# Optimization experiments

Hardware: AMD Instinct MI355X
Metric: run time of the kernel (lower is better)

Reference implementation:

```python
import jax, jax.numpy as jnp
import numpy as np

D, H, DH = 768, 12, 64
W = 256            # one-sided window (attention_window=512 total)
EPS = 1e-6
NEG = -1e9


def layer_norm(x, g, b):
    m = jnp.mean(x, axis=-1, keepdims=True)
    v = jnp.mean((x - m) ** 2, axis=-1, keepdims=True)
    return g * (x - m) * jax.lax.rsqrt(v + EPS) + b


def _blocks3(t, nb):
    # t: [B,H,nb,W,dh] -> keys/values of 3 neighboring blocks [B,H,nb,3W,dh]
    tp = jnp.pad(t, ((0, 0), (0, 0), (1, 1), (0, 0), (0, 0)))
    return jnp.concatenate([tp[:, :, :nb], tp[:, :, 1:nb + 1], tp[:, :, 2:nb + 2]], axis=3)


def sliding_window_attention(x, kpm, Wq, bq, Wk, bk, Wv, bv, Wo, bo):
    B, S, _ = x.shape
    nb = S // W
    def proj(Wm, bm):
        return (x @ Wm + bm).reshape(B, S, H, DH).transpose(0, 2, 1, 3).reshape(B, H, nb, W, DH)
    q = proj(Wq, bq) * (1.0 / np.sqrt(DH))
    k = proj(Wk, bk)
    v = proj(Wv, bv)
    k3 = _blocks3(k, nb)
    v3 = _blocks3(v, nb)
    # scores over local band: [B,H,nb,W,3W]
    s = jnp.einsum('bhnqd,bhnkd->bhnqk', q, k3)
    qi = jnp.arange(W)[:, None]
    kj = jnp.arange(3 * W)[None, :]
    band = jnp.abs(kj - W - qi) <= W                     # [W,3W]
    kg = (jnp.arange(nb)[:, None, None] - 1) * W + kj[None]  # global key idx [nb,1,3W]
    inrange = (kg >= 0) & (kg < S)
    # key padding mask gathered into block layout: [B,nb,3W]
    kpm_b = jnp.pad(kpm.reshape(B, nb, W), ((0, 0), (1, 1), (0, 0)), constant_values=True)
    kpm3 = jnp.concatenate([kpm_b[:, :nb], kpm_b[:, 1:nb + 1], kpm_b[:, 2:nb + 2]], axis=2)
    m = band[None, None, None] & inrange[None, None] & (~kpm3)[:, None, :, None, :]
    s = jnp.where(m, s, NEG)
    p = jax.nn.softmax(s, axis=-1)
    o = jnp.einsum('bhnqk,bhnkd->bhnqd', p, v3)
    o = o.reshape(B, H, S, DH).transpose(0, 2, 1, 3).reshape(B, S, D)
    return o @ Wo + bo


def setup_inputs() -> dict:
    key = jax.random.key(0)
    ks = jax.random.split(key, 12)
    B, S, DF = 2, 4096, 3072
    sc = 1.0 / np.sqrt(D)
    return {
        'x': jax.random.normal(ks[0], (B, S, D), jnp.float32),
        'mask': jnp.zeros((B, S), bool),
        'id': 0,
        'Wq': jax.random.normal(ks[1], (D, D), jnp.float32) * sc,
        'bq': jnp.zeros((D,), jnp.float32),
        'Wk': jax.random.normal(ks[2], (D, D), jnp.float32) * sc,
        'bk': jnp.zeros((D,), jnp.float32),
        'Wv': jax.random.normal(ks[3], (D, D), jnp.float32) * sc,
        'bv': jnp.zeros((D,), jnp.float32),
        'Wo': jax.random.normal(ks[4], (D, D), jnp.float32) * sc,
        'bo': jnp.zeros((D,), jnp.float32),
        'ln1_g': jnp.ones((D,), jnp.float32),
        'ln1_b': jnp.zeros((D,), jnp.float32),
        'W1': jax.random.normal(ks[5], (D, DF), jnp.float32) * sc,
        'b1': jnp.zeros((DF,), jnp.float32),
        'W2': jax.random.normal(ks[6], (DF, D), jnp.float32) * (1.0 / np.sqrt(DF)),
        'b2': jnp.zeros((D,), jnp.float32),
        'ln2_g': jnp.ones((D,), jnp.float32),
        'ln2_b': jnp.zeros((D,), jnp.float32),
    }


def reference(x, mask, id, Wq, bq, Wk, bk, Wv, bv, Wo, bo, ln1_g, ln1_b, W1, b1, W2, b2, ln2_g, ln2_b):
    # Sublayer 1: pre-norm residual around sliding-window self-attention
    h = layer_norm(x, ln1_g, ln1_b)
    x = x + sliding_window_attention(h, mask, Wq, bq, Wk, bk, Wv, bv, Wo, bo)
    # Sublayer 2: pre-norm residual around positionwise FFN
    h = layer_norm(x, ln2_g, ln2_b)
    x = x + (jax.nn.relu(h @ W1 + b1) @ W2 + b2)
    return x
```

## Files before the change

### kernel.cpp

```cpp
#include <hip/hip_runtime.h>
#include <hip/hip_bf16.h>
#include <cstddef>

typedef __attribute__((ext_vector_type(8))) short short8;
typedef __attribute__((ext_vector_type(4))) float f32x4;
typedef __attribute__((ext_vector_type(4))) unsigned short us4;

typedef __attribute__((address_space(1))) void as1_void;
typedef __attribute__((address_space(3))) void as3_void;

__device__ __forceinline__ void gload16(const void* g, void* lds) {
  __builtin_amdgcn_global_load_lds((as1_void*)(void*)g, (as3_void*)lds, 16, 0, 0);
}

__device__ inline unsigned short f2bf(float f) {
  union { float f; unsigned int u; } v; v.f = f;
  return (unsigned short)((v.u + 0x7FFFu + ((v.u >> 16) & 1u)) >> 16);
}

__device__ __forceinline__ float exp2v(float x) {
  float r; asm("v_exp_f32 %0, %1" : "=v"(r) : "v"(x)); return r;
}
__device__ __forceinline__ unsigned cvtpk(float a, float b) {
  unsigned r; asm("v_cvt_pk_bf16_f32 %0, %1, %2" : "=v"(r) : "v"(a), "v"(b)); return r;
}

__global__ __launch_bounds__(256) void ln_kernel(const float* __restrict__ x,
    const float* __restrict__ g, const float* __restrict__ b,
    unsigned short* __restrict__ out)
{
  int row = blockIdx.x, t = threadIdx.x;
  const float* xr = x + (size_t)row * 768;
  float v0 = xr[t], v1 = xr[t + 256], v2 = xr[t + 512];
  float s = v0 + v1 + v2;
  #pragma unroll
  for (int o = 32; o > 0; o >>= 1) s += __shfl_xor(s, o);
  __shared__ float r1[4], r2[4];
  if ((t & 63) == 0) r1[t >> 6] = s;
  __syncthreads();
  float mean = (r1[0] + r1[1] + r1[2] + r1[3]) * (1.0f / 768.0f);
  float d0 = v0 - mean, d1 = v1 - mean, d2 = v2 - mean;
  float q = d0 * d0 + d1 * d1 + d2 * d2;
  #pragma unroll
  for (int o = 32; o > 0; o >>= 1) q += __shfl_xor(q, o);
  if ((t & 63) == 0) r2[t >> 6] = q;
  __syncthreads();
  float var = (r2[0] + r2[1] + r2[2] + r2[3]) * (1.0f / 768.0f);
  float rs = rsqrtf(var + 1e-6f);
  unsigned short* orow = out + (size_t)row * 768;
  orow[t]       = f2bf(g[t]       * d0 * rs + b[t]);
  orow[t + 256] = f2bf(g[t + 256] * d1 * rs + b[t + 256]);
  orow[t + 512] = f2bf(g[t + 512] * d2 * rs + b[t + 512]);
}

__global__ __launch_bounds__(256) void transpose_kernel(const float* __restrict__ W,
    unsigned short* __restrict__ WT, int K, int N)
{
  __shared__ float tile[32][33];
  int tx = threadIdx.x & 31, ty = threadIdx.x >> 5;
  int k0 = blockIdx.x * 32, n0 = blockIdx.y * 32;
  #pragma unroll
  for (int i = 0; i < 32; i += 8)
    tile[ty + i][tx] = W[(size_t)(k0 + ty + i) * N + n0 + tx];
  __syncthreads();
  #pragma unroll
  for (int i = 0; i < 32; i += 8)
    WT[(size_t)(n0 + ty + i) * K + k0 + tx] = f2bf(tile[tx][ty + i]);
}

__global__ __launch_bounds__(256) void catbias_kernel(const float* __restrict__ bq,
    const float* __restrict__ bk, const float* __restrict__ bv, float* __restrict__ o)
{
  int i = blockIdx.x * 256 + threadIdx.x;
  o[i] = (i < 768) ? bq[i] : ((i < 1536) ? bk[i - 768] : bv[i - 1536]);
}

enum { EPI_QKV = 0, EPI_RELU = 1, EPI_RESID = 2 };

template<int EPI>
__global__ __launch_bounds__(512, 1) void gemmP_kernel(
    const unsigned short* __restrict__ A, const unsigned short* __restrict__ BT,
    const float* __restrict__ bias, const float* __restrict__ resid,
    void* __restrict__ outp, int M, int N, int K, int ntn)
{
  __shared__ char lds[3][49152];
  int tid = threadIdx.x;
  int nwg = gridDim.x;
  int bid = ((int)blockIdx.x & 7) * (nwg >> 3) + ((int)blockIdx.x >> 3);
  int mt = bid / ntn, nt = bid % ntn;
  int m0 = mt * 128, n0 = nt * 256;
  int w = tid >> 6, l = tid & 63;
  int wr = w >> 2, wc = w & 3;
  int fr = l & 15, fq = l >> 4;
  int swz = (fr >> 1) * 128 + (((((fr & 1) << 2) | fq) ^ ((fr >> 1) & 7)) << 4);
  int t8 = tid >> 3;
  int uu = (tid & 7) ^ (t8 & 7);
  int rb = 2 * t8 + (uu >> 2);
  int kb = (uu & 3) * 8;
  const unsigned short* Asrc  = A  + (size_t)(m0 + rb) * K + kb;
  const unsigned short* Bsrc0 = BT + (size_t)(n0 + rb) * K + kb;
  const unsigned short* Bsrc1 = BT + (size_t)(n0 + 128 + rb) * K + kb;

  auto stage = [&](int buf, int kt, int h) {
    int ko = kt * 64 + h * 32;
    char* dA = &lds[buf][0] + h * 8192 + (w << 10);
    char* dB = &lds[buf][16384] + h * 16384 + (w << 10);
    gload16(Asrc + ko, dA);
    gload16(Bsrc0 + ko, dB);
    gload16(Bsrc1 + ko, dB + 8192);
  };

  f32x4 acc[4][4] = {};

#define GP_COMPUTE(RBUF, H)                                                    \
  { short8 af[4], bf[4];                                                       \
    const char* ab_ = &lds[RBUF][0] + (H) * 8192 + wr * 4096 + swz;            \
    const char* bb_ = &lds[RBUF][16384] + (H) * 16384 + wc * 4096 + swz;       \
    _Pragma("unroll")                                                          \
    for (int i_ = 0; i_ < 4; i_++) af[i_] = *(const short8*)(ab_ + i_ * 1024); \
    _Pragma("unroll")                                                          \
    for (int j_ = 0; j_ < 4; j_++) bf[j_] = *(const short8*)(bb_ + j_ * 1024); \
    __builtin_amdgcn_s_setprio(1);                                             \
    _Pragma("unroll")                                                          \
    for (int i_ = 0; i_ < 4; i_++)                                             \
      _Pragma("unroll")                                                        \
      for (int j_ = 0; j_ < 4; j_++)                                           \
        acc[i_][j_] = __builtin_amdgcn_mfma_f32_16x16x32_bf16(                 \
            af[i_], bf[j_], acc[i_][j_], 0, 0, 0);                             \
    __builtin_amdgcn_s_setprio(0); }

  stage(0, 0, 0); stage(0, 0, 1); stage(1, 1, 0); stage(1, 1, 1);
  asm volatile("s_waitcnt vmcnt(9)" ::: "memory");
  __builtin_amdgcn_s_barrier();

  int NT = K >> 6;
  int R = 0;
  for (int t = 0; t < NT - 2; ++t) {
    int W = (R == 0) ? 2 : R - 1;
    stage(W, t + 2, 0);
    GP_COMPUTE(R, 0);
    asm volatile("s_waitcnt vmcnt(9)" ::: "memory");
    __builtin_amdgcn_s_barrier();
    stage(W, t + 2, 1);
    GP_COMPUTE(R, 1);
    asm volatile("s_waitcnt vmcnt(9)" ::: "memory");
    __builtin_amdgcn_s_barrier();
    R = (R == 2) ? 0 : R + 1;
  }
  GP_COMPUTE(R, 0);
  asm volatile("s_waitcnt vmcnt(6)" ::: "memory");
  __builtin_amdgcn_s_barrier();
  GP_COMPUTE(R, 1);
  asm volatile("s_waitcnt vmcnt(3)" ::: "memory");
  __builtin_amdgcn_s_barrier();
  R = (R == 2) ? 0 : R + 1;
  GP_COMPUTE(R, 0);
  asm volatile("s_waitcnt vmcnt(0)" ::: "memory");
  __builtin_amdgcn_s_barrier();
  GP_COMPUTE(R, 1);
#undef GP_COMPUTE

  #pragma unroll
  for (int nj = 0; nj < 4; nj++) {
    int col = n0 + wc * 64 + nj * 16 + fr;
    float bs = bias[col];
    if (EPI == EPI_QKV) {
      int which = (col >= 1536) ? 2 : ((col >= 768) ? 1 : 0);
      int c2 = col - which * 768;
      int hh = c2 >> 6, dh = c2 & 63;
      if (which == 2) {
        unsigned short* dstv = reinterpret_cast<unsigned short*>(outp) + (size_t)2 * 8192 * 768;
        #pragma unroll
        for (int i = 0; i < 4; i++) {
          int row0 = m0 + wr * 64 + i * 16 + fq * 4;
          int bb = row0 >> 12, sl = row0 & 4095;
          us4 pv;
          #pragma unroll
          for (int r = 0; r < 4; r++) pv[r] = f2bf(acc[i][nj][r] + bs);
          *reinterpret_cast<us4*>(&dstv[((size_t)(bb * 12 + hh) * 64 + dh) * 4096 + sl]) = pv;
        }
      } else {
        unsigned short* dst = reinterpret_cast<unsigned short*>(outp) + (size_t)which * 8192 * 768;
        #pragma unroll
        for (int i = 0; i < 4; i++) {
          #pragma unroll
          for (int r = 0; r < 4; r++) {
            int row = m0 + wr * 64 + i * 16 + fq * 4 + r;
            float c = acc[i][nj][r] + bs;
            if (which == 0) c *= 0.18033688011112042f;
            int bb = row >> 12, sl = row & 4095;
            dst[(((size_t)(bb * 12 + hh)) * 4096 + sl) * 64 + dh] = f2bf(c);
          }
        }
      }
    } else if (EPI == EPI_RELU) {
      #pragma unroll
      for (int i = 0; i < 4; i++)
        #pragma unroll
        for (int r = 0; r < 4; r++) {
          int row = m0 + wr * 64 + i * 16 + fq * 4 + r;
          float c = fmaxf(acc[i][nj][r] + bs, 0.0f);
          reinterpret_cast<unsigned short*>(outp)[(size_t)row * N + col] = f2bf(c);
        }
    } else {
      #pragma unroll
      for (int i = 0; i < 4; i++)
        #pragma unroll
        for (int r = 0; r < 4; r++) {
          int row = m0 + wr * 64 + i * 16 + fq * 4 + r;
          float c = acc[i][nj][r] + bs + resid[(size_t)row * N + col];
          reinterpret_cast<float*>(outp)[(size_t)row * N + col] = c;
        }
    }
  }
}

__global__ __launch_bounds__(256) void attn_fused_kernel(
    const unsigned short* __restrict__ qg, const unsigned short* __restrict__ kg,
    const unsigned short* __restrict__ vtg, const unsigned char* __restrict__ kpm,
    unsigned short* __restrict__ attn_out)
{
  __shared__ unsigned short lds_k[2][64 * 64];
  __shared__ unsigned short lds_vt[2][64 * 64];
  __shared__ unsigned short lds_p[4][32 * 64];
  int bid0 = blockIdx.x;
  int bid = (bid0 & 7) * 96 + (bid0 >> 3);
  int qblk = bid & 31, h = (bid >> 5) % 12, b = bid / 384;
  int bh = b * 12 + h;
  int q0 = qblk * 128;
  int tid = threadIdx.x, w = tid >> 6, l = tid & 63;
  int fr = l & 15, fq = l >> 4;
  int qw0 = q0 + w * 32;
  int swzb = (((l & 7) ^ (l >> 3)) << 4);
  const char* qbase  = (const char*)(qg  + (size_t)bh * 4096 * 64);
  const char* kbase  = (const char*)(kg  + (size_t)bh * 4096 * 64);
  const char* vtbase = (const char*)(vtg + (size_t)bh * 64 * 4096);
  const unsigned char* kpmb = kpm + (size_t)b * 4096;

  #pragma unroll
  for (int s = 0; s < 4; s++) {
    int row = w * 32 + s * 8 + (l >> 3);
    gload16(qbase + (size_t)(q0 + row) * 128 + swzb, (char*)lds_p[w] + s * 1024);
  }

  auto stageKV = [&](int c, int buf) {
    int g0 = q0 - 256 + c * 64;
    if (g0 < 0 || g0 >= 4096) return;
    #pragma unroll
    for (int s = 0; s < 2; s++) {
      int row = w * 16 + s * 8 + (l >> 3);
      gload16(kbase + (size_t)(g0 + row) * 128 + swzb,
              (char*)lds_k[buf] + (w * 2 + s) * 1024);
      gload16(vtbase + ((size_t)row * 4096 + g0) * 2 + swzb,
              (char*)lds_vt[buf] + (w * 2 + s) * 1024);
    }
  };

  stageKV(0, 0);
  asm volatile("s_waitcnt vmcnt(0)");
  __syncthreads();

  short8 qf[2][2];
  #pragma unroll
  for (int i = 0; i < 2; i++)
    #pragma unroll
    for (int ks = 0; ks < 2; ks++)
      qf[i][ks] = *(const short8*)((const char*)lds_p[w] + (i * 16 + fr) * 128 +
                    ((ks * 64 + fq * 16) ^ ((fr & 7) << 4)));

  f32x4 acc_o[2][4] = {};
  float m_st[2] = {-3.0e38f, -3.0e38f};
  float l_st[2] = {0.0f, 0.0f};

  for (int c = 0; c < 10; c++) {
    int g0 = q0 - 256 + c * 64;
    bool valid = (g0 >= 0) && (g0 < 4096);
    if (c < 9) stageKV(c + 1, (c + 1) & 1);
    if (valid) {
      int buf = c & 1;
      unsigned int km[4];
      #pragma unroll
      for (int j = 0; j < 4; j++)
        km[j] = *(const unsigned int*)(kpmb + g0 + 16 * j + 4 * fq);
      bool anyk = __any((km[0] | km[1] | km[2] | km[3]) != 0);
      int rel = g0 - qw0;
      bool edge = anyk || (rel < -225) || (rel > 193);
      short8 kf[4][2];
      #pragma unroll
      for (int j = 0; j < 4; j++)
        #pragma unroll
        for (int ks = 0; ks < 2; ks++)
          kf[j][ks] = *(const short8*)((const char*)lds_k[buf] + (j * 16 + fr) * 128 +
                        ((ks * 64 + fq * 16) ^ ((fr & 7) << 4)));
      f32x4 accs[4][2] = {};
      #pragma unroll
      for (int j = 0; j < 4; j++)
        #pragma unroll
        for (int i = 0; i < 2; i++)
          #pragma unroll
          for (int ks = 0; ks < 2; ks++)
            accs[j][i] = __builtin_amdgcn_mfma_f32_16x16x32_bf16(kf[j][ks], qf[i][ks], accs[j][i], 0, 0, 0);
      #pragma unroll
      for (int i = 0; i < 2; i++) {
        float sv[4][4];
        #pragma unroll
        for (int j = 0; j < 4; j++)
          #pragma unroll
          for (int r = 0; r < 4; r++)
            sv[j][r] = accs[j][i][r];
        if (edge) {
          int base = rel + 4 * fq - fr - 16 * i;
          #pragma unroll
          for (int j = 0; j < 4; j++)
            #pragma unroll
            for (int r = 0; r < 4; r++) {
              int d = base + 16 * j + r;
              bool ok = (d >= -256) && (d <= 256) && (((km[j] >> (8 * r)) & 255u) == 0u);
              if (!ok) sv[j][r] = -1.0e9f;
            }
        }
        float mv = sv[0][0];
        #pragma unroll
        for (int j = 0; j < 4; j++)
          #pragma unroll
          for (int r = 0; r < 4; r++) mv = fmaxf(mv, sv[j][r]);
        mv = fmaxf(mv, __shfl_xor(mv, 16));
        mv = fmaxf(mv, __shfl_xor(mv, 32));
        float mo = m_st[i];
        if (!__all(mv - mo <= 8.0f)) {
          float mn = fmaxf(mo, mv);
          float scl = exp2v(mo - mn);
          l_st[i] *= scl;
          m_st[i] = mn;
          #pragma unroll
          for (int r = 0; r < 4; r++) {
            float so = __shfl(scl, (l & 48) | ((l >> 2) & 12) | r);
            #pragma unroll
            for (int jd = 0; jd < 4; jd++) acc_o[i][jd][r] *= so;
          }
        }
        float mn = m_st[i];
        float rs = 0.0f;
        char* prow = (char*)lds_p[w] + (i * 16 + fr) * 128;
        #pragma unroll
        for (int j = 0; j < 4; j++) {
          float p0 = exp2v(sv[j][0] - mn), p1 = exp2v(sv[j][1] - mn);
          float p2 = exp2v(sv[j][2] - mn), p3 = exp2v(sv[j][3] - mn);
          rs += (p0 + p1) + (p2 + p3);
          uint2 u; u.x = cvtpk(p0, p1); u.y = cvtpk(p2, p3);
          *(uint2*)(prow + ((32 * j + 8 * fq) ^ ((fr & 7) << 4))) = u;
        }
        rs += __shfl_xor(rs, 16);
        rs += __shfl_xor(rs, 32);
        l_st[i] += rs;
      }
      short8 pf[2][2];
      #pragma unroll
      for (int i = 0; i < 2; i++)
        #pragma unroll
        for (int ks = 0; ks < 2; ks++)
          pf[i][ks] = *(const short8*)((const char*)lds_p[w] + (i * 16 + fr) * 128 +
                        ((ks * 64 + fq * 16) ^ ((fr & 7) << 4)));
      short8 vf[4][2];
      #pragma unroll
      for (int jd = 0; jd < 4; jd++)
        #pragma unroll
        for (int ks = 0; ks < 2; ks++)
          vf[jd][ks] = *(const short8*)((const char*)lds_vt[buf] + (jd * 16 + fr) * 128 +
                        ((ks * 64 + fq * 16) ^ ((fr & 7) << 4)));
      #pragma unroll
      for (int i = 0; i < 2; i++)
        #pragma unroll
        for (int jd = 0; jd < 4; jd++)
          #pragma unroll
          for (int ks = 0; ks < 2; ks++)
            acc_o[i][jd] = __builtin_amdgcn_mfma_f32_16x16x32_bf16(pf[i][ks], vf[jd][ks], acc_o[i][jd], 0, 0, 0);
    }
    asm volatile("s_waitcnt vmcnt(0)");
    __syncthreads();
  }
  #pragma unroll
  for (int i = 0; i < 2; i++) {
    #pragma unroll
    for (int r = 0; r < 4; r++) {
      float lv = __shfl(l_st[i], (l & 48) | ((l >> 2) & 12) | r);
      float inv = 1.0f / lv;
      int qrow = qw0 + i * 16 + fq * 4 + r;
      size_t orow = ((size_t)b * 4096 + qrow) * 768 + h * 64;
      #pragma unroll
      for (int jd = 0; jd < 4; jd++)
        attn_out[orow + jd * 16 + fr] = f2bf(acc_o[i][jd][r] * inv);
    }
  }
}

extern "C" void kernel_launch(void* const* d_in, const int* in_sizes, int n_in,
                              void* d_out, int out_size, void* d_ws, size_t ws_size,
                              hipStream_t stream) {
  const float* x            = (const float*)d_in[0];
  const unsigned char* mask = (const unsigned char*)d_in[1];
  const float* Wq  = (const float*)d_in[3];
  const float* bq  = (const float*)d_in[4];
  const float* Wk  = (const float*)d_in[5];
  const float* bk  = (const float*)d_in[6];
  const float* Wv  = (const float*)d_in[7];
  const float* bv  = (const float*)d_in[8];
  const float* Wo  = (const float*)d_in[9];
  const float* bo  = (const float*)d_in[10];
  const float* ln1g = (const float*)d_in[11];
  const float* ln1b = (const float*)d_in[12];
  const float* W1  = (const float*)d_in[13];
  const float* b1  = (const float*)d_in[14];
  const float* W2  = (const float*)d_in[15];
  const float* b2  = (const float*)d_in[16];
  const float* ln2g = (const float*)d_in[17];
  const float* ln2b = (const float*)d_in[18];
  float* out = (float*)d_out;

  char* ws = (char*)d_ws;
  size_t off = 0;
  auto alloc = [&](size_t bytes) -> void* {
    void* p = ws + off;
    off += (bytes + 255) & ~(size_t)255;
    return p;
  };
  unsigned short* WTqkv = (unsigned short*)alloc((size_t)2304 * 768 * 2);
  unsigned short* WTo   = (unsigned short*)alloc((size_t)768 * 768 * 2);
  unsigned short* W1T   = (unsigned short*)alloc((size_t)3072 * 768 * 2);
  unsigned short* W2T   = (unsigned short*)alloc((size_t)768 * 3072 * 2);
  float*          bqkv  = (float*)alloc(2304 * 4);
  unsigned short* hbuf  = (unsigned short*)alloc((size_t)8192 * 768 * 2);
  unsigned short* qkv   = (unsigned short*)alloc((size_t)3 * 8192 * 768 * 2);
  unsigned short* attn  = (unsigned short*)alloc((size_t)8192 * 768 * 2);
  float* x1             = (float*)alloc((size_t)8192 * 768 * 4);
  unsigned short* h2    = (unsigned short*)alloc((size_t)8192 * 768 * 2);
  unsigned short* a1    = (unsigned short*)alloc((size_t)8192 * 3072 * 2);

  transpose_kernel<<<dim3(24, 24), 256, 0, stream>>>(Wq, WTqkv, 768, 768);
  transpose_kernel<<<dim3(24, 24), 256, 0, stream>>>(Wk, WTqkv + (size_t)768 * 768, 768, 768);
  transpose_kernel<<<dim3(24, 24), 256, 0, stream>>>(Wv, WTqkv + (size_t)1536 * 768, 768, 768);
  transpose_kernel<<<dim3(24, 24), 256, 0, stream>>>(Wo, WTo, 768, 768);
  transpose_kernel<<<dim3(24, 96), 256, 0, stream>>>(W1, W1T, 768, 3072);
  transpose_kernel<<<dim3(96, 24), 256, 0, stream>>>(W2, W2T, 3072, 768);
  catbias_kernel<<<9, 256, 0, stream>>>(bq, bk, bv, bqkv);

  ln_kernel<<<8192, 256, 0, stream>>>(x, ln1g, ln1b, hbuf);

  gemmP_kernel<EPI_QKV><<<576, 512, 0, stream>>>(hbuf, WTqkv, bqkv, nullptr, qkv, 8192, 2304, 768, 9);

  attn_fused_kernel<<<768, 256, 0, stream>>>(qkv, qkv + (size_t)8192 * 768,
                                             qkv + (size_t)2 * 8192 * 768, mask, attn);

  gemmP_kernel<EPI_RESID><<<192, 512, 0, stream>>>(attn, WTo, bo, x, x1, 8192, 768, 768, 3);
  ln_kernel<<<8192, 256, 0, stream>>>(x1, ln2g, ln2b, h2);
  gemmP_kernel<EPI_RELU><<<768, 512, 0, stream>>>(h2, W1T, b1, nullptr, a1, 8192, 3072, 768, 12);
  gemmP_kernel<EPI_RESID><<<192, 512, 0, stream>>>(a1, W2T, b2, x1, out, 8192, 768, 3072, 3);
}
```

Baseline: 265.8 us.

## Merge weight prep launches and deepen attention and GEMM prefetch pipelines

Merges the six weight transpose launches and the bias concat into one prep kernel, which removes six launches. The GEMM main loop is reorganised so each phase waits, reads its LDS fragments, issues the next global-to-LDS stage, then barriers before the MFMAs. This lets the loads overlap with compute more cleanly, at the cost of an extra barrier per phase. The attention kernel moves from double to triple buffering of K/V tiles with vmcnt-based waits, removing the full vmcnt(0) wait plus syncthreads at the end of each chunk. It adds LDS use and relies on the vmcnt counting being correct.

```diff
diff --git a/kernel.cpp b/kernel.cpp
--- a/kernel.cpp
+++ b/kernel.cpp
@@ -53,12 +53,33 @@
   orow[t + 512] = f2bf(g[t + 512] * d2 * rs + b[t + 512]);
 }
 
-__global__ __launch_bounds__(256) void transpose_kernel(const float* __restrict__ W,
-    unsigned short* __restrict__ WT, int K, int N)
+__global__ __launch_bounds__(256) void prep_kernel(
+    const float* __restrict__ Wq, const float* __restrict__ Wk,
+    const float* __restrict__ Wv, const float* __restrict__ Wo,
+    const float* __restrict__ W1, const float* __restrict__ W2,
+    const float* __restrict__ bq, const float* __restrict__ bk,
+    const float* __restrict__ bv,
+    unsigned short* __restrict__ WTqkv, unsigned short* __restrict__ WTo,
+    unsigned short* __restrict__ W1T, unsigned short* __restrict__ W2T,
+    float* __restrict__ bqkv)
 {
+  int bid = blockIdx.x;
+  if (bid >= 6912) {
+    int i = (bid - 6912) * 256 + threadIdx.x;
+    bqkv[i] = (i < 768) ? bq[i] : ((i < 1536) ? bk[i - 768] : bv[i - 1536]);
+    return;
+  }
+  const float* W; unsigned short* WT; int K, N, lb;
+  if (bid < 576)       { W = Wq; WT = WTqkv;                        K = 768;  N = 768;  lb = bid; }
+  else if (bid < 1152) { W = Wk; WT = WTqkv + (size_t)768 * 768;    K = 768;  N = 768;  lb = bid - 576; }
+  else if (bid < 1728) { W = Wv; WT = WTqkv + (size_t)1536 * 768;   K = 768;  N = 768;  lb = bid - 1152; }
+  else if (bid < 2304) { W = Wo; WT = WTo;                          K = 768;  N = 768;  lb = bid - 1728; }
+  else if (bid < 4608) { W = W1; WT = W1T;                          K = 768;  N = 3072; lb = bid - 2304; }
+  else                 { W = W2; WT = W2T;                          K = 3072; N = 768;  lb = bid - 4608; }
+  int ntN = N >> 5;
+  int k0 = (lb / ntN) * 32, n0 = (lb % ntN) * 32;
   __shared__ float tile[32][33];
   int tx = threadIdx.x & 31, ty = threadIdx.x >> 5;
-  int k0 = blockIdx.x * 32, n0 = blockIdx.y * 32;
   #pragma unroll
   for (int i = 0; i < 32; i += 8)
     tile[ty + i][tx] = W[(size_t)(k0 + ty + i) * N + n0 + tx];
@@ -66,13 +87,6 @@
   #pragma unroll
   for (int i = 0; i < 32; i += 8)
     WT[(size_t)(n0 + ty + i) * K + k0 + tx] = f2bf(tile[tx][ty + i]);
-}
-
-__global__ __launch_bounds__(256) void catbias_kernel(const float* __restrict__ bq,
-    const float* __restrict__ bk, const float* __restrict__ bv, float* __restrict__ o)
-{
-  int i = blockIdx.x * 256 + threadIdx.x;
-  o[i] = (i < 768) ? bq[i] : ((i < 1536) ? bk[i - 768] : bv[i - 1536]);
 }
 
 enum { EPI_QKV = 0, EPI_RELU = 1, EPI_RESID = 2 };
@@ -111,54 +125,53 @@
   };
 
   f32x4 acc[4][4] = {};
-
-#define GP_COMPUTE(RBUF, H)                                                    \
-  { short8 af[4], bf[4];                                                       \
-    const char* ab_ = &lds[RBUF][0] + (H) * 8192 + wr * 4096 + swz;            \
+  short8 af[4], bf[4];
+
+#define GP_READ(RBUF, H)                                                       \
+  { const char* ab_ = &lds[RBUF][0] + (H) * 8192 + wr * 4096 + swz;            \
     const char* bb_ = &lds[RBUF][16384] + (H) * 16384 + wc * 4096 + swz;       \
     _Pragma("unroll")                                                          \
     for (int i_ = 0; i_ < 4; i_++) af[i_] = *(const short8*)(ab_ + i_ * 1024); \
     _Pragma("unroll")                                                          \
-    for (int j_ = 0; j_ < 4; j_++) bf[j_] = *(const short8*)(bb_ + j_ * 1024); \
-    __builtin_amdgcn_s_setprio(1);                                             \
+    for (int j_ = 0; j_ < 4; j_++) bf[j_] = *(const short8*)(bb_ + j_ * 1024); }
+
+#define GP_MFMA                                                                \
+  __builtin_amdgcn_s_setprio(1);                                               \
+  _Pragma("unroll")                                                            \
+  for (int i_ = 0; i_ < 4; i_++)                                               \
     _Pragma("unroll")                                                          \
-    for (int i_ = 0; i_ < 4; i_++)                                             \
-      _Pragma("unroll")                                                        \
-      for (int j_ = 0; j_ < 4; j_++)                                           \
-        acc[i_][j_] = __builtin_amdgcn_mfma_f32_16x16x32_bf16(                 \
-            af[i_], bf[j_], acc[i_][j_], 0, 0, 0);                             \
-    __builtin_amdgcn_s_setprio(0); }
+    for (int j_ = 0; j_ < 4; j_++)                                             \
+      acc[i_][j_] = __builtin_amdgcn_mfma_f32_16x16x32_bf16(                   \
+          af[i_], bf[j_], acc[i_][j_], 0, 0, 0);                               \
+  __builtin_amdgcn_s_setprio(0);
+
+#define GP_PHASE(VN, RBUF, H, DOSTAGE, WBUF, KT)                               \
+  asm volatile("s_waitcnt vmcnt(" #VN ")" ::: "memory");                       \
+  __builtin_amdgcn_s_barrier();                                                \
+  GP_READ(RBUF, H);                                                            \
+  if (DOSTAGE) stage(WBUF, KT, H);                                             \
+  asm volatile("" ::: "memory");                                               \
+  __builtin_amdgcn_s_barrier();                                                \
+  GP_MFMA;
 
   stage(0, 0, 0); stage(0, 0, 1); stage(1, 1, 0); stage(1, 1, 1);
-  asm volatile("s_waitcnt vmcnt(9)" ::: "memory");
-  __builtin_amdgcn_s_barrier();
 
   int NT = K >> 6;
   int R = 0;
   for (int t = 0; t < NT - 2; ++t) {
     int W = (R == 0) ? 2 : R - 1;
-    stage(W, t + 2, 0);
-    GP_COMPUTE(R, 0);
-    asm volatile("s_waitcnt vmcnt(9)" ::: "memory");
-    __builtin_amdgcn_s_barrier();
-    stage(W, t + 2, 1);
-    GP_COMPUTE(R, 1);
-    asm volatile("s_waitcnt vmcnt(9)" ::: "memory");
-    __builtin_amdgcn_s_barrier();
+    GP_PHASE(9, R, 0, 1, W, t + 2);
+    GP_PHASE(9, R, 1, 1, W, t + 2);
     R = (R == 2) ? 0 : R + 1;
   }
-  GP_COMPUTE(R, 0);
-  asm volatile("s_waitcnt vmcnt(6)" ::: "memory");
-  __builtin_amdgcn_s_barrier();
-  GP_COMPUTE(R, 1);
-  asm volatile("s_waitcnt vmcnt(3)" ::: "memory");
-  __builtin_amdgcn_s_barrier();
+  GP_PHASE(9, R, 0, 0, 0, 0);
+  GP_PHASE(6, R, 1, 0, 0, 0);
   R = (R == 2) ? 0 : R + 1;
-  GP_COMPUTE(R, 0);
-  asm volatile("s_waitcnt vmcnt(0)" ::: "memory");
-  __builtin_amdgcn_s_barrier();
-  GP_COMPUTE(R, 1);
-#undef GP_COMPUTE
+  GP_PHASE(3, R, 0, 0, 0, 0);
+  GP_PHASE(0, R, 1, 0, 0, 0);
+#undef GP_PHASE
+#undef GP_MFMA
+#undef GP_READ
 
   #pragma unroll
   for (int nj = 0; nj < 4; nj++) {
@@ -220,8 +233,8 @@
     const unsigned short* __restrict__ vtg, const unsigned char* __restrict__ kpm,
     unsigned short* __restrict__ attn_out)
 {
-  __shared__ unsigned short lds_k[2][64 * 64];
-  __shared__ unsigned short lds_vt[2][64 * 64];
+  __shared__ unsigned short lds_k[3][64 * 64];
+  __shared__ unsigned short lds_vt[3][64 * 64];
   __shared__ unsigned short lds_p[4][32 * 64];
   int bid0 = blockIdx.x;
   int bid = (bid0 & 7) * 96 + (bid0 >> 3);
@@ -255,10 +268,23 @@
               (char*)lds_vt[buf] + (w * 2 + s) * 1024);
     }
   };
-
-  stageKV(0, 0);
-  asm volatile("s_waitcnt vmcnt(0)");
-  __syncthreads();
+  auto stageKVc = [&](int c, int buf) {
+    int g0 = q0 - 256 + c * 64;
+    g0 = (g0 < 0) ? 0 : ((g0 > 4032) ? 4032 : g0);
+    #pragma unroll
+    for (int s = 0; s < 2; s++) {
+      int row = w * 16 + s * 8 + (l >> 3);
+      gload16(kbase + (size_t)(g0 + row) * 128 + swzb,
+              (char*)lds_k[buf] + (w * 2 + s) * 1024);
+      gload16(vtbase + ((size_t)row * 4096 + g0) * 2 + swzb,
+              (char*)lds_vt[buf] + (w * 2 + s) * 1024);
+    }
+  };
+  (void)stageKV;
+
+  stageKVc(0, 0);
+  stageKVc(1, 1);
+  asm volatile("s_waitcnt vmcnt(8)" ::: "memory");
 
   short8 qf[2][2];
   #pragma unroll
@@ -273,11 +299,14 @@
   float l_st[2] = {0.0f, 0.0f};
 
   for (int c = 0; c < 10; c++) {
+    if (c < 9) { asm volatile("s_waitcnt vmcnt(4)" ::: "memory"); }
+    else       { asm volatile("s_waitcnt vmcnt(0)" ::: "memory"); }
+    __builtin_amdgcn_s_barrier();
+    if (c < 8) stageKVc(c + 2, (c + 2) % 3);
     int g0 = q0 - 256 + c * 64;
     bool valid = (g0 >= 0) && (g0 < 4096);
-    if (c < 9) stageKV(c + 1, (c + 1) & 1);
     if (valid) {
-      int buf = c & 1;
+      int buf = c % 3;
       unsigned int km[4];
       #pragma unroll
       for (int j = 0; j < 4; j++)
@@ -376,8 +405,6 @@
           for (int ks = 0; ks < 2; ks++)
             acc_o[i][jd] = __builtin_amdgcn_mfma_f32_16x16x32_bf16(pf[i][ks], vf[jd][ks], acc_o[i][jd], 0, 0, 0);
     }
-    asm volatile("s_waitcnt vmcnt(0)");
-    __syncthreads();
   }
   #pragma unroll
   for (int i = 0; i < 2; i++) {
@@ -436,13 +463,8 @@
   unsigned short* h2    = (unsigned short*)alloc((size_t)8192 * 768 * 2);
   unsigned short* a1    = (unsigned short*)alloc((size_t)8192 * 3072 * 2);
 
-  transpose_kernel<<<dim3(24, 24), 256, 0, stream>>>(Wq, WTqkv, 768, 768);
-  transpose_kernel<<<dim3(24, 24), 256, 0, stream>>>(Wk, WTqkv + (size_t)768 * 768, 768, 768);
-  transpose_kernel<<<dim3(24, 24), 256, 0, stream>>>(Wv, WTqkv + (size_t)1536 * 768, 768, 768);
-  transpose_kernel<<<dim3(24, 24), 256, 0, stream>>>(Wo, WTo, 768, 768);
-  transpose_kernel<<<dim3(24, 96), 256, 0, stream>>>(W1, W1T, 768, 3072);
-  transpose_kernel<<<dim3(96, 24), 256, 0, stream>>>(W2, W2T, 3072, 768);
-  catbias_kernel<<<9, 256, 0, stream>>>(bq, bk, bv, bqkv);
+  prep_kernel<<<6921, 256, 0, stream>>>(Wq, Wk, Wv, Wo, W1, W2, bq, bk, bv,
+                                        WTqkv, WTo, W1T, W2T, bqkv);
 
   ln_kernel<<<8192, 256, 0, stream>>>(x, ln1g, ln1b, hbuf);
 
```

New measurement: 259.4 us. 2.4% less time.
